# Performance work log

Measured on AMD Instinct MI355X. Metric: run time of the kernel, lower is better.

The kernel has to match this reference:

```python
import jax, jax.numpy as jnp
import numpy as np

B, S, T, H, V = 32, 64, 64, 512, 32000


def setup_inputs() -> dict:
    key = jax.random.key(0)
    ks = jax.random.split(key, 14)
    enc = jax.random.normal(ks[0], (B, S, H), jnp.float32)
    h0 = jax.random.normal(ks[1], (1, B, H), jnp.float32)
    # encoder padding mask: at least half of each row valid (avoids all -inf rows)
    src_len = jax.random.randint(ks[2], (B,), S // 2, S + 1)
    enc_mask = (jnp.arange(S)[None, :] < src_len[:, None])
    tgt = jax.random.randint(ks[3], (B, T), 0, V)
    fra_len = jax.random.randint(ks[4], (B,), 1, T + 1).at[0].set(T)
    s = 1.0 / np.sqrt(H)
    emb = jax.random.normal(ks[5], (V, H), jnp.float32) * s
    W_ih = jax.random.uniform(ks[6], (3 * H, H), jnp.float32, -s, s)
    W_hh = jax.random.uniform(ks[7], (3 * H, H), jnp.float32, -s, s)
    b_ih = jax.random.uniform(ks[8], (3 * H,), jnp.float32, -s, s)
    b_hh = jax.random.uniform(ks[9], (3 * H,), jnp.float32, -s, s)
    W_cc = jax.random.uniform(ks[10], (H, 2 * H), jnp.float32, -s, s)
    b_cc = jnp.zeros((H,), jnp.float32)
    W_out = jax.random.uniform(ks[11], (V, H), jnp.float32, -s, s)
    b_out = jnp.zeros((V,), jnp.float32)
    return {"all_encoder_hidden_states": enc, "initial_decoder_hidden_state": h0,
            "encoder_output_mask": enc_mask, "target_input": tgt, "fra_length": fra_len,
            "embedding": emb, "W_ih": W_ih, "W_hh": W_hh, "b_ih": b_ih, "b_hh": b_hh,
            "W_cc": W_cc, "b_cc": b_cc, "W_out": W_out, "b_out": b_out}


def reference(all_encoder_hidden_states, initial_decoder_hidden_state, encoder_output_mask,
              target_input, fra_length, embedding, W_ih, W_hh, b_ih, b_hh,
              W_cc, b_cc, W_out, b_out):
    enc = all_encoder_hidden_states            # [B,S,H]
    mask = encoder_output_mask                 # [B,S] bool
    xs = embedding[target_input].transpose(1, 0, 2)  # [T,B,H]
    ts = jnp.arange(xs.shape[0])

    def step(h, inp):                          # h: [B,H]
        x, t = inp
        gx = x @ W_ih.T + b_ih                 # [B,3H]
        gh = h @ W_hh.T + b_hh
        gxr, gxz, gxn = jnp.split(gx, 3, axis=-1)
        ghr, ghz, ghn = jnp.split(gh, 3, axis=-1)
        r = jax.nn.sigmoid(gxr + ghr)
        z = jax.nn.sigmoid(gxz + ghz)
        n = jnp.tanh(gxn + r * ghn)
        h_new = (1.0 - z) * n + z * h          # torch GRU update
        # Luong dot-product attention
        scores = jnp.einsum('bsh,bh->bs', enc, h_new)
        scores = jnp.where(mask, scores, -jnp.inf)
        alphas = jax.nn.softmax(scores, axis=-1)
        ctx = jnp.einsum('bs,bsh->bh', alphas, enc)
        ho = jnp.tanh(jnp.concatenate([ctx, h_new], axis=-1) @ W_cc.T + b_cc)
        logit = ho @ W_out.T + b_out           # [B,V]
        active = (t < fra_length)[:, None]
        h_next = jnp.where(active, h_new, h)   # freeze finished sequences
        return h_next, logit

    _, logits = jax.lax.scan(step, initial_decoder_hidden_state[0], (xs, ts))
    logits = logits.transpose(1, 0, 2)          # [B,T,V]
    return jax.nn.log_softmax(logits, axis=-1)
```

## Files before the change

### kernel.cpp

```cpp
#include <hip/hip_runtime.h>

static constexpr int Bn = 32, Sn = 64, Tn = 64, Hn = 512, Vn = 32000;
static constexpr int H3 = 1536;

typedef __attribute__((ext_vector_type(8))) short bf16x8;
typedef __attribute__((ext_vector_type(4))) float f32x4;

__device__ __forceinline__ short f2bf(float f) {
    unsigned u = __float_as_uint(f);
    u += 0x7FFFu + ((u >> 16) & 1u);
    return (short)(u >> 16);
}
__device__ __forceinline__ float bf2f(short s) {
    return __uint_as_float(((unsigned)(unsigned short)s) << 16);
}

__device__ __forceinline__ void gload16(const void* g, void* l) {
    __builtin_amdgcn_global_load_lds(
        (const __attribute__((address_space(1))) unsigned int*)g,
        (__attribute__((address_space(3))) unsigned int*)l, 16, 0, 0);
}

__global__ __launch_bounds__(256) void k_prep(const int* __restrict__ tgt,
                                              const float* __restrict__ emb,
                                              const float* __restrict__ W_ih,
                                              const float* __restrict__ W_hh,
                                              const float* __restrict__ W_cc,
                                              short* __restrict__ Xb,
                                              short* __restrict__ Wih_b, short* __restrict__ Whh_b,
                                              short* __restrict__ Wc1_b, short* __restrict__ Wc2_b) {
    const int bid = blockIdx.x, tid = threadIdx.x;
    if (bid < 2048) {
        long u = (long)bid * 256 + tid;
        const float* src; short* dst;
        if (u < 196608)       { long e = u * 4;            src = W_ih + e; dst = Wih_b + e; }
        else if (u < 393216)  { long e = (u - 196608) * 4; src = W_hh + e; dst = Whh_b + e; }
        else if (u < 458752)  { long e = (u - 393216) * 4; long r = e >> 9; int c = (int)(e & 511);
                                src = W_cc + r * 1024 + c;       dst = Wc1_b + e; }
        else                  { long e = (u - 458752) * 4; long r = e >> 9; int c = (int)(e & 511);
                                src = W_cc + r * 1024 + 512 + c; dst = Wc2_b + e; }
        const float4 v = *(const float4*)src;
        short4 o; o.x = f2bf(v.x); o.y = f2bf(v.y); o.z = f2bf(v.z); o.w = f2bf(v.w);
        *(short4*)dst = o;
    } else {
        const int m = (bid - 2048) * 2 + (tid >> 7);
        const int c = (tid & 127) * 4;
        const float4 v = *(const float4*)(emb + (long)tgt[m] * Hn + c);
        short4 o; o.x = f2bf(v.x); o.y = f2bf(v.y); o.z = f2bf(v.z); o.w = f2bf(v.w);
        *(short4*)(Xb + (long)m * Hn + c) = o;
    }
}

__global__ __launch_bounds__(256) void k_gemm_bf16(const short* __restrict__ A, int lda,
                                                   const short* __restrict__ Bm, int ldb,
                                                   const float* __restrict__ bias,
                                                   float* __restrict__ C, int ldc, int K) {
    __shared__ short lA[4096];
    __shared__ short lB[4096];
    const int tid = threadIdx.x;
    const int row0 = blockIdx.y * 128;
    const int col0 = blockIdx.x * 128;
    const int lane = tid & 63;
    const int w = tid >> 6;
    const int wr = w >> 1, wc = w & 1;
    const int g = lane >> 4, rr = lane & 15;

    f32x4 acc[4][4];
    for (int m = 0; m < 4; ++m)
        for (int n = 0; n < 4; ++n)
            for (int q = 0; q < 4; ++q) acc[m][n][q] = 0.f;

    for (int kk = 0; kk < K; kk += 32) {
        for (int p = 0; p < 2; ++p) {
            int u = p * 256 + tid;
            int kg = u >> 7, r = u & 127;
            gload16(A + (long)(row0 + r) * lda + kk + kg * 8, &lA[u * 8]);
            gload16(Bm + (long)(col0 + r) * ldb + kk + kg * 8, &lB[u * 8]);
        }
        __syncthreads();
        bf16x8 av[4], bv[4];
        for (int m = 0; m < 4; ++m)
            av[m] = *(const bf16x8*)&lA[(g * 128 + wr * 64 + m * 16 + rr) * 8];
        for (int n = 0; n < 4; ++n)
            bv[n] = *(const bf16x8*)&lB[(g * 128 + wc * 64 + n * 16 + rr) * 8];
        for (int m = 0; m < 4; ++m)
            for (int n = 0; n < 4; ++n)
                acc[m][n] = __builtin_amdgcn_mfma_f32_16x16x32_bf16(av[m], bv[n], acc[m][n], 0, 0, 0);
        __syncthreads();
    }

    for (int n = 0; n < 4; ++n) {
        int gc = col0 + wc * 64 + n * 16 + rr;
        float bb = bias ? bias[gc] : 0.f;
        for (int m = 0; m < 4; ++m) {
            int gr = row0 + wr * 64 + m * 16 + g * 4;
            for (int q = 0; q < 4; ++q)
                C[(long)(gr + q) * ldc + gc] = acc[m][n][q] + bb;
        }
    }
}

__global__ __launch_bounds__(256) void k_gemm_logits(const short* __restrict__ A,
                                                     const short* __restrict__ Bm,
                                                     const float* __restrict__ bias,
                                                     float* __restrict__ Cf,
                                                     short* __restrict__ Cb,
                                                     float* __restrict__ stats,
                                                     int use_bf16) {
    __shared__ short lA[4096];
    __shared__ short lB[4096];
    __shared__ float sml[128][2];
    __shared__ float ssl[128][2];
    const int tid = threadIdx.x;
    const int row0 = blockIdx.y * 128;
    const int col0 = blockIdx.x * 128;
    const int lane = tid & 63;
    const int w = tid >> 6;
    const int wr = w >> 1, wc = w & 1;
    const int g = lane >> 4, rr = lane & 15;

    f32x4 acc[4][4];
    for (int m = 0; m < 4; ++m)
        for (int n = 0; n < 4; ++n)
            for (int q = 0; q < 4; ++q) acc[m][n][q] = 0.f;

    for (int kk = 0; kk < 512; kk += 32) {
        for (int p = 0; p < 2; ++p) {
            int u = p * 256 + tid;
            int kg = u >> 7, r = u & 127;
            gload16(A + (long)(row0 + r) * 512 + kk + kg * 8, &lA[u * 8]);
            gload16(Bm + (long)(col0 + r) * 512 + kk + kg * 8, &lB[u * 8]);
        }
        __syncthreads();
        bf16x8 av[4], bv[4];
        for (int m = 0; m < 4; ++m)
            av[m] = *(const bf16x8*)&lA[(g * 128 + wr * 64 + m * 16 + rr) * 8];
        for (int n = 0; n < 4; ++n)
            bv[n] = *(const bf16x8*)&lB[(g * 128 + wc * 64 + n * 16 + rr) * 8];
        for (int m = 0; m < 4; ++m)
            for (int n = 0; n < 4; ++n)
                acc[m][n] = __builtin_amdgcn_mfma_f32_16x16x32_bf16(av[m], bv[n], acc[m][n], 0, 0, 0);
        __syncthreads();
    }

    float bb[4];
    #pragma unroll
    for (int n = 0; n < 4; ++n) bb[n] = bias[col0 + wc * 64 + n * 16 + rr];

    if (use_bf16) {
        #pragma unroll
        for (int n = 0; n < 4; ++n) {
            int gc = col0 + wc * 64 + n * 16 + rr;
            #pragma unroll
            for (int m = 0; m < 4; ++m) {
                int gr = row0 + wr * 64 + m * 16 + g * 4;
                #pragma unroll
                for (int q = 0; q < 4; ++q)
                    Cb[(long)(gr + q) * Vn + gc] = f2bf(acc[m][n][q] + bb[n]);
            }
        }
    } else {
        #pragma unroll
        for (int n = 0; n < 4; ++n) {
            int gc = col0 + wc * 64 + n * 16 + rr;
            #pragma unroll
            for (int m = 0; m < 4; ++m) {
                int gr = row0 + wr * 64 + m * 16 + g * 4;
                #pragma unroll
                for (int q = 0; q < 4; ++q)
                    Cf[(long)(gr + q) * Vn + gc] = acc[m][n][q] + bb[n];
            }
        }
    }
    #pragma unroll
    for (int m = 0; m < 4; ++m) {
        #pragma unroll
        for (int q = 0; q < 4; ++q) {
            float mx = acc[m][0][q] + bb[0];
            mx = fmaxf(mx, acc[m][1][q] + bb[1]);
            mx = fmaxf(mx, acc[m][2][q] + bb[2]);
            mx = fmaxf(mx, acc[m][3][q] + bb[3]);
            mx = fmaxf(mx, __shfl_xor(mx, 1));
            mx = fmaxf(mx, __shfl_xor(mx, 2));
            mx = fmaxf(mx, __shfl_xor(mx, 4));
            mx = fmaxf(mx, __shfl_xor(mx, 8));
            float s = __expf(acc[m][0][q] + bb[0] - mx) + __expf(acc[m][1][q] + bb[1] - mx)
                    + __expf(acc[m][2][q] + bb[2] - mx) + __expf(acc[m][3][q] + bb[3] - mx);
            s += __shfl_xor(s, 1);
            s += __shfl_xor(s, 2);
            s += __shfl_xor(s, 4);
            s += __shfl_xor(s, 8);
            if (rr == 0) {
                const int r = wr * 64 + m * 16 + g * 4 + q;
                sml[r][wc] = mx; ssl[r][wc] = s;
            }
        }
    }
    __syncthreads();
    if (tid < 128) {
        const float m0 = sml[tid][0], m1 = sml[tid][1];
        const float mm = fmaxf(m0, m1);
        const float ss = ssl[tid][0] * __expf(m0 - mm) + ssl[tid][1] * __expf(m1 - mm);
        float2* sp = (float2*)stats;
        sp[(long)(row0 + tid) * 256 + blockIdx.x] = make_float2(mm, ss);
    }
}

__global__ __launch_bounds__(256) void k_sub(float* __restrict__ out, const short* __restrict__ Cb,
                                             const float* __restrict__ stats, int use_bf16) {
    const long row = blockIdx.x;
    const int tid = threadIdx.x;
    __shared__ float lse_s;
    if (tid < 64) {
        float m = -__builtin_inff(), s = 0.f;
        for (int tc = tid; tc < 250; tc += 64) {
            const float2 p = ((const float2*)stats)[row * 256 + tc];
            const float nm = fmaxf(m, p.x);
            s = s * __expf(m - nm) + p.y * __expf(p.x - nm);
            m = nm;
        }
        for (int o = 1; o < 64; o <<= 1) {
            const float om = __shfl_xor(m, o), os = __shfl_xor(s, o);
            const float nm = fmaxf(m, om);
            s = s * __expf(m - nm) + os * __expf(om - nm);
            m = nm;
        }
        if (tid == 0) lse_s = m + logf(s);
    }
    __syncthreads();
    const float lse = lse_s;
    float* p = out + row * (long)Vn;
    if (use_bf16) {
        const short* cp = Cb + row * (long)Vn;
        for (int i = tid; i < Vn / 4; i += 256) {
            short4 c = *(const short4*)(cp + i * 4);
            float4 v;
            v.x = bf2f(c.x) - lse; v.y = bf2f(c.y) - lse;
            v.z = bf2f(c.z) - lse; v.w = bf2f(c.w) - lse;
            *(float4*)(p + i * 4) = v;
        }
    } else {
        for (int i = tid; i < Vn / 4; i += 256) {
            float4 v = *(const float4*)(p + i * 4);
            v.x -= lse; v.y -= lse; v.z -= lse; v.w -= lse;
            *(float4*)(p + i * 4) = v;
        }
    }
}

__global__ __launch_bounds__(256) void k_ho(const short* __restrict__ A1, const short* __restrict__ A2,
                                            const short* __restrict__ B1, const short* __restrict__ B2,
                                            const float* __restrict__ bias, short* __restrict__ C) {
    __shared__ short lA[4096];
    __shared__ short lB[4096];
    const int tid = threadIdx.x;
    const int row0 = blockIdx.y * 128;
    const int col0 = blockIdx.x * 128;
    const int lane = tid & 63;
    const int w = tid >> 6;
    const int wr = w >> 1, wc = w & 1;
    const int g = lane >> 4, rr = lane & 15;

    f32x4 acc[4][4];
    for (int m = 0; m < 4; ++m)
        for (int n = 0; n < 4; ++n)
            for (int q = 0; q < 4; ++q) acc[m][n][q] = 0.f;

    for (int ph = 0; ph < 2; ++ph) {
        const short* A = ph ? A2 : A1;
        const short* Bm = ph ? B2 : B1;
        for (int kk = 0; kk < 512; kk += 32) {
            for (int p = 0; p < 2; ++p) {
                int u = p * 256 + tid;
                int kg = u >> 7, r = u & 127;
                gload16(A + (long)(row0 + r) * 512 + kk + kg * 8, &lA[u * 8]);
                gload16(Bm + (long)(col0 + r) * 512 + kk + kg * 8, &lB[u * 8]);
            }
            __syncthreads();
            bf16x8 av[4], bv[4];
            for (int m = 0; m < 4; ++m)
                av[m] = *(const bf16x8*)&lA[(g * 128 + wr * 64 + m * 16 + rr) * 8];
            for (int n = 0; n < 4; ++n)
                bv[n] = *(const bf16x8*)&lB[(g * 128 + wc * 64 + n * 16 + rr) * 8];
            for (int m = 0; m < 4; ++m)
                for (int n = 0; n < 4; ++n)
                    acc[m][n] = __builtin_amdgcn_mfma_f32_16x16x32_bf16(av[m], bv[n], acc[m][n], 0, 0, 0);
            __syncthreads();
        }
    }

    for (int n = 0; n < 4; ++n) {
        int gc = col0 + wc * 64 + n * 16 + rr;
        float bb = bias[gc];
        for (int m = 0; m < 4; ++m) {
            int gr = row0 + wr * 64 + m * 16 + g * 4;
            for (int q = 0; q < 4; ++q)
                C[(long)(gr + q) * 512 + gc] = f2bf(tanhf(acc[m][n][q] + bb));
        }
    }
}

struct WSm3 {
    short h_all[Bn * Hn];
    float gh_sl[3 * 16 * 32];
};
struct ASm3 {
    short encl[Sn * 520];
    float scp[8][64];
    float al[64];
    short hnf[Hn];
};
union USm3 { WSm3 w; ASm3 a; };

__device__ __forceinline__ void sig_flag(unsigned* slot, unsigned val) {
    asm volatile("s_waitcnt vmcnt(0)" ::: "memory");
    __syncthreads();
    if (threadIdx.x == 0)
        __hip_atomic_store(slot, val, __ATOMIC_RELAXED, __HIP_MEMORY_SCOPE_AGENT);
}
__device__ __forceinline__ void wait_flags32(const unsigned* base, unsigned need) {
    if (threadIdx.x < 32) {
        while (__hip_atomic_load(base + threadIdx.x * 32, __ATOMIC_RELAXED, __HIP_MEMORY_SCOPE_AGENT) < need)
            __builtin_amdgcn_s_sleep(1);
    }
    __syncthreads();
}

__global__ __launch_bounds__(512, 1) void k_seq(
    const float* __restrict__ GX, const int* __restrict__ fra,
    const float* __restrict__ h0,
    const short* __restrict__ Whh_b, const float* __restrict__ b_hh,
    const float* __restrict__ enc, const void* __restrict__ maskp,
    unsigned long long* __restrict__ hn_pk,
    short* __restrict__ ctx_b,
    unsigned long long* __restrict__ hn_pub,
    unsigned* __restrict__ flags,
    const float* __restrict__ W_out, short* __restrict__ Wout_b)
{
    __shared__ __align__(16) USm3 sm;
    const int bid = blockIdx.x;
    const int tid = threadIdx.x;

    if (bid >= 64) {
        const long base = (long)(bid - 64) * (512 * 16);
        #pragma unroll
        for (int it = 0; it < 16; ++it) {
            long i = base + it * 512 + tid;
            if (i < (long)Vn * Hn / 4) {
                const float4 v = *(const float4*)(W_out + i * 4);
                short4 o; o.x = f2bf(v.x); o.y = f2bf(v.y); o.z = f2bf(v.z); o.w = f2bf(v.w);
                *(short4*)(Wout_b + i * 4) = o;
            }
        }
        return;
    }

    const int wv = tid >> 6, lane = tid & 63;

    if (bid >= Bn) {
        const int b = bid - Bn;
        const unsigned w0 = ((const unsigned*)maskp)[0];
        const int mmode = (w0 == 1u) ? 0 : (w0 == 0x3F800000u ? 2 : 1);
        {
            const float* encb = enc + (long)b * (Sn * Hn);
            #pragma unroll
            for (int it = 0; it < 16; ++it) {
                int e = (it * 512 + tid) * 4;
                float4 v = *(const float4*)(encb + e);
                int s = e >> 9, k = e & 511;
                short4 o; o.x = f2bf(v.x); o.y = f2bf(v.y); o.z = f2bf(v.z); o.w = f2bf(v.w);
                *(short4*)(sm.a.encl + s * 520 + k) = o;
            }
        }
        __syncthreads();
        for (int u = 0; u < Tn; ++u) {
            wait_flags32(flags, (unsigned)(u + 1));
            if (tid < 128) {
                unsigned long long v = __hip_atomic_load(hn_pk + (long)(b * Tn + u) * 128 + tid,
                                                         __ATOMIC_RELAXED, __HIP_MEMORY_SCOPE_AGENT);
                *(unsigned long long*)&sm.a.hnf[tid * 4] = v;
            }
            __syncthreads();
            {
                const int s = tid & 63, sub = tid >> 6;
                const short* erow = sm.a.encl + s * 520 + sub * 64;
                const short* hrow = sm.a.hnf + sub * 64;
                float p = 0.f;
                #pragma unroll
                for (int c8 = 0; c8 < 8; ++c8) {
                    bf16x8 ev = *(const bf16x8*)(erow + c8 * 8);
                    bf16x8 hv8 = *(const bf16x8*)(hrow + c8 * 8);
                    #pragma unroll
                    for (int e = 0; e < 8; ++e)
                        p += bf2f(ev[e]) * bf2f(hv8[e]);
                }
                sm.a.scp[sub][s] = p;
            }
            __syncthreads();
            if (tid < 64) {
                float v = 0.f;
                #pragma unroll
                for (int q = 0; q < 8; ++q) v += sm.a.scp[q][tid];
                bool mv;
                if (mmode == 0)      mv = ((const int*)maskp)[b * Sn + tid] != 0;
                else if (mmode == 1) mv = ((const unsigned char*)maskp)[b * Sn + tid] != 0;
                else                 mv = ((const float*)maskp)[b * Sn + tid] != 0.f;
                v = mv ? v : -__builtin_inff();
                float mx = v;
                for (int o = 1; o < 64; o <<= 1) mx = fmaxf(mx, __shfl_xor(mx, o));
                float e = __expf(v - mx);
                float su = e;
                for (int o = 1; o < 64; o <<= 1) su += __shfl_xor(su, o);
                sm.a.al[tid] = e / su;
            }
            __syncthreads();
            {
                float cx = 0.f;
                #pragma unroll 8
                for (int s = 0; s < 64; ++s)
                    cx += sm.a.al[s] * bf2f(sm.a.encl[s * 520 + tid]);
                ctx_b[(long)(b * Tn + u) * Hn + tid] = f2bf(cx);
            }
        }
        return;
    }

    bf16x8 afr[16];
    if (wv < 6) {
        const int g = wv >> 1;
        const int row = g * 512 + bid * 16 + (lane & 15);
        #pragma unroll
        for (int k = 0; k < 16; ++k)
            afr[k] = *(const bf16x8*)(Whh_b + (long)row * 512 + k * 32 + (lane >> 4) * 8);
    }
    #pragma unroll
    for (int it = 0; it < 8; ++it) {
        const int idx2 = it * 512 + tid;
        const int b = idx2 >> 7, ci2 = idx2 & 127;
        const int j0 = ci2 * 4;
        const int soff = b * 512 + ((((ci2 >> 1)) ^ (b & 7)) << 3) + (ci2 & 1) * 4;
        const float4 v = *(const float4*)(h0 + b * 512 + j0);
        unsigned long long pk = (unsigned long long)(unsigned short)f2bf(v.x)
                              | ((unsigned long long)(unsigned short)f2bf(v.y) << 16)
                              | ((unsigned long long)(unsigned short)f2bf(v.z) << 32)
                              | ((unsigned long long)(unsigned short)f2bf(v.w) << 48);
        *(unsigned long long*)&sm.w.h_all[soff] = pk;
    }

    const int eb = tid >> 4, jj = tid & 15;
    float h_carry = h0[eb * 512 + bid * 16 + jj];
    const int flen_e = fra[eb];
    const int jglob = bid * 16 + jj;
    const float bhr = b_hh[jglob];
    const float bhz = b_hh[512 + jglob];
    const float bhn = b_hh[1024 + jglob];

    const int ci2s = wv * 16 + (lane & 15);
    const unsigned* fp = flags + (ci2s >> 2) * 32;
    const int bbase = lane >> 4;

    for (int t = 0; t < Tn; ++t) {
        const long base = (long)(eb * Tn + t) * H3 + jglob;
        const float gxr = GX[base];
        const float gxz = GX[base + 512];
        const float gxn = GX[base + 1024];
        if (t >= 1) {
            while (__hip_atomic_load(fp, __ATOMIC_RELAXED, __HIP_MEMORY_SCOPE_AGENT) < (unsigned)t)
                __builtin_amdgcn_s_sleep(1);
            const unsigned long long* src = hn_pub + ((t - 1) & 1) * 4096;
            #pragma unroll
            for (int it = 0; it < 8; ++it) {
                const int b = bbase + it * 4;
                const unsigned long long v =
                    __hip_atomic_load(src + b * 128 + ci2s, __ATOMIC_RELAXED, __HIP_MEMORY_SCOPE_AGENT);
                const int soff = b * 512 + ((((ci2s >> 1)) ^ (b & 7)) << 3) + (ci2s & 1) * 4;
                *(unsigned long long*)&sm.w.h_all[soff] = v;
            }
        }
        __syncthreads();
        if (wv < 6) {
            const int g = wv >> 1, n = wv & 1;
            const int bq = n * 16 + (lane & 15);
            f32x4 a0 = {0.f, 0.f, 0.f, 0.f}, a1 = {0.f, 0.f, 0.f, 0.f};
            #pragma unroll
            for (int k = 0; k < 8; ++k) {
                const int c0 = k * 4 + (lane >> 4);
                const int c1 = (k + 8) * 4 + (lane >> 4);
                bf16x8 b0 = *(const bf16x8*)&sm.w.h_all[bq * 512 + ((c0 ^ (bq & 7)) << 3)];
                bf16x8 b1 = *(const bf16x8*)&sm.w.h_all[bq * 512 + ((c1 ^ (bq & 7)) << 3)];
                a0 = __builtin_amdgcn_mfma_f32_16x16x32_bf16(afr[k], b0, a0, 0, 0, 0);
                a1 = __builtin_amdgcn_mfma_f32_16x16x32_bf16(afr[k + 8], b1, a1, 0, 0, 0);
            }
            const int r0 = (lane >> 4) * 4;
            #pragma unroll
            for (int q = 0; q < 4; ++q)
                sm.w.gh_sl[g * 512 + (r0 + q) * 32 + bq] = a0[q] + a1[q];
        }
        __syncthreads();
        {
            const float ghr = sm.w.gh_sl[jj * 32 + eb]          + bhr;
            const float ghz = sm.w.gh_sl[512 + jj * 32 + eb]    + bhz;
            const float ghn = sm.w.gh_sl[1024 + jj * 32 + eb]   + bhn;
            const float r = 1.f / (1.f + __expf(-(gxr + ghr)));
            const float z = 1.f / (1.f + __expf(-(gxz + ghz)));
            const float nn = tanhf(gxn + r * ghn);
            const float hv = (1.f - z) * nn + z * h_carry;
            h_carry = (t < flen_e) ? hv : h_carry;
            int f32w = (int)(unsigned short)f2bf(h_carry);
            int r32w = (int)(unsigned short)f2bf(hv);
            int f1 = __shfl_down(f32w, 1), f2 = __shfl_down(f32w, 2), f3 = __shfl_down(f32w, 3);
            int r1 = __shfl_down(r32w, 1), r2 = __shfl_down(r32w, 2), r3 = __shfl_down(r32w, 3);
            if ((jj & 3) == 0) {
                unsigned long long pkf = (unsigned long long)(unsigned)(f32w | (f1 << 16))
                                       | ((unsigned long long)(unsigned)(f2 | (f3 << 16)) << 32);
                unsigned long long pkr = (unsigned long long)(unsigned)(r32w | (r1 << 16))
                                       | ((unsigned long long)(unsigned)(r2 | (r3 << 16)) << 32);
                __hip_atomic_store(hn_pub + (t & 1) * 4096 + eb * 128 + bid * 4 + (jj >> 2), pkf,
                                   __ATOMIC_RELAXED, __HIP_MEMORY_SCOPE_AGENT);
                __hip_atomic_store(hn_pk + (long)(eb * Tn + t) * 128 + bid * 4 + (jj >> 2), pkr,
                                   __ATOMIC_RELAXED, __HIP_MEMORY_SCOPE_AGENT);
            }
            sig_flag(flags + bid * 32, (unsigned)(t + 1));
        }
    }
}

extern "C" void kernel_launch(void* const* d_in, const int* in_sizes, int n_in,
                              void* d_out, int out_size, void* d_ws, size_t ws_size,
                              hipStream_t stream) {
    const float* enc   = (const float*)d_in[0];
    const float* h0    = (const float*)d_in[1];
    const void*  maskp = d_in[2];
    const int*   tgt   = (const int*)d_in[3];
    const int*   fra   = (const int*)d_in[4];
    const float* emb   = (const float*)d_in[5];
    const float* W_ih  = (const float*)d_in[6];
    const float* W_hh  = (const float*)d_in[7];
    const float* b_ih  = (const float*)d_in[8];
    const float* b_hh  = (const float*)d_in[9];
    const float* W_cc  = (const float*)d_in[10];
    const float* b_cc  = (const float*)d_in[11];
    const float* W_out = (const float*)d_in[12];
    const float* b_out = (const float*)d_in[13];
    float* out = (float*)d_out;

    char* ws = (char*)d_ws;
    float*    GX      = (float*)ws;   ws += (long)2048 * 1536 * 4;
    short*    Xb      = (short*)ws;   ws += (long)2048 * 512 * 2;
    short*    Wih_b   = (short*)ws;   ws += (long)1536 * 512 * 2;
    short*    Wout_b  = (short*)ws;   ws += (long)32000 * 512 * 2;
    short*    Whh_b   = (short*)ws;   ws += (long)1536 * 512 * 2;
    short*    Wc1_b   = (short*)ws;   ws += (long)512 * 512 * 2;
    short*    Wcc2_b  = (short*)ws;   ws += (long)512 * 512 * 2;
    short*    ho_b    = (short*)ws;   ws += (long)2048 * 512 * 2;
    short*    hn_all  = (short*)ws;   ws += (long)2048 * 512 * 2;
    short*    ctx_b   = (short*)ws;   ws += (long)2048 * 512 * 2;
    float*    stats   = (float*)ws;   ws += (long)2048 * 256 * 2 * 4;
    unsigned long long* hn_pub = (unsigned long long*)ws; ws += (long)2 * 4096 * 8;
    unsigned* flags   = (unsigned*)ws; ws += 1024 * 4;
    const long cb_bytes = (long)2048 * Vn * 2;
    const long used = (long)(ws - (char*)d_ws);
    const int use_bf16 = (ws_size >= (size_t)(used + cb_bytes)) ? 1 : 0;
    short* Cb = use_bf16 ? (short*)ws : nullptr;

    hipMemsetAsync(flags, 0, 1024 * 4, stream);
    k_prep<<<3072, 256, 0, stream>>>(tgt, emb, W_ih, W_hh, W_cc, Xb, Wih_b, Whh_b, Wc1_b, Wcc2_b);

    k_gemm_bf16<<<dim3(12, 16), 256, 0, stream>>>(Xb, 512, Wih_b, 512, b_ih, GX, 1536, 512);

    k_seq<<<576, 512, 0, stream>>>(GX, fra, h0, Whh_b, b_hh, enc, maskp,
                                   (unsigned long long*)hn_all, ctx_b, hn_pub, flags,
                                   W_out, Wout_b);

    k_ho<<<dim3(4, 16), 256, 0, stream>>>(ctx_b, hn_all, Wc1_b, Wcc2_b, b_cc, ho_b);

    k_gemm_logits<<<dim3(250, 16), 256, 0, stream>>>(ho_b, Wout_b, b_out, out, Cb, stats, use_bf16);

    k_sub<<<2048, 256, 0, stream>>>(out, Cb, stats, use_bf16);
}
```

Measured before the change: 676.0 us.

## Fuse combine-projection and logits GEMM into persistent sequential kernel with flag pipelining

Removes the separate k_ho and k_gemm_logits launches. Attention blocks now compute the tanh(W_cc·[ctx,h]) projection every four timesteps and publish ho rows with flags. 192 extra persistent blocks convert W_out to bf16 and then run the vocabulary logits GEMM tiles as soon as each 128-row chunk of ho is ready, so the large GEMM overlaps the recurrent GRU loop. Rows are reordered time-major, with index remapping in k_sub and stats. This adds spin-wait synchronisation and relies on co-residency of all 256 blocks, and the GEMM tiles may contend with the latency-critical recurrence.

```diff
diff --git a/kernel.cpp b/kernel.cpp
--- a/kernel.cpp
+++ b/kernel.cpp
@@ -28,17 +28,14 @@
                                               const float* __restrict__ W_cc,
                                               short* __restrict__ Xb,
                                               short* __restrict__ Wih_b, short* __restrict__ Whh_b,
-                                              short* __restrict__ Wc1_b, short* __restrict__ Wc2_b) {
+                                              short* __restrict__ Wcc_b) {
     const int bid = blockIdx.x, tid = threadIdx.x;
     if (bid < 2048) {
         long u = (long)bid * 256 + tid;
         const float* src; short* dst;
         if (u < 196608)       { long e = u * 4;            src = W_ih + e; dst = Wih_b + e; }
         else if (u < 393216)  { long e = (u - 196608) * 4; src = W_hh + e; dst = Whh_b + e; }
-        else if (u < 458752)  { long e = (u - 393216) * 4; long r = e >> 9; int c = (int)(e & 511);
-                                src = W_cc + r * 1024 + c;       dst = Wc1_b + e; }
-        else                  { long e = (u - 458752) * 4; long r = e >> 9; int c = (int)(e & 511);
-                                src = W_cc + r * 1024 + 512 + c; dst = Wc2_b + e; }
+        else                  { long e = (u - 393216) * 4; src = W_cc + e; dst = Wcc_b + e; }
         const float4 v = *(const float4*)src;
         short4 o; o.x = f2bf(v.x); o.y = f2bf(v.y); o.z = f2bf(v.z); o.w = f2bf(v.w);
         *(short4*)dst = o;
@@ -100,112 +97,6 @@
     }
 }
 
-__global__ __launch_bounds__(256) void k_gemm_logits(const short* __restrict__ A,
-                                                     const short* __restrict__ Bm,
-                                                     const float* __restrict__ bias,
-                                                     float* __restrict__ Cf,
-                                                     short* __restrict__ Cb,
-                                                     float* __restrict__ stats,
-                                                     int use_bf16) {
-    __shared__ short lA[4096];
-    __shared__ short lB[4096];
-    __shared__ float sml[128][2];
-    __shared__ float ssl[128][2];
-    const int tid = threadIdx.x;
-    const int row0 = blockIdx.y * 128;
-    const int col0 = blockIdx.x * 128;
-    const int lane = tid & 63;
-    const int w = tid >> 6;
-    const int wr = w >> 1, wc = w & 1;
-    const int g = lane >> 4, rr = lane & 15;
-
-    f32x4 acc[4][4];
-    for (int m = 0; m < 4; ++m)
-        for (int n = 0; n < 4; ++n)
-            for (int q = 0; q < 4; ++q) acc[m][n][q] = 0.f;
-
-    for (int kk = 0; kk < 512; kk += 32) {
-        for (int p = 0; p < 2; ++p) {
-            int u = p * 256 + tid;
-            int kg = u >> 7, r = u & 127;
-            gload16(A + (long)(row0 + r) * 512 + kk + kg * 8, &lA[u * 8]);
-            gload16(Bm + (long)(col0 + r) * 512 + kk + kg * 8, &lB[u * 8]);
-        }
-        __syncthreads();
-        bf16x8 av[4], bv[4];
-        for (int m = 0; m < 4; ++m)
-            av[m] = *(const bf16x8*)&lA[(g * 128 + wr * 64 + m * 16 + rr) * 8];
-        for (int n = 0; n < 4; ++n)
-            bv[n] = *(const bf16x8*)&lB[(g * 128 + wc * 64 + n * 16 + rr) * 8];
-        for (int m = 0; m < 4; ++m)
-            for (int n = 0; n < 4; ++n)
-                acc[m][n] = __builtin_amdgcn_mfma_f32_16x16x32_bf16(av[m], bv[n], acc[m][n], 0, 0, 0);
-        __syncthreads();
-    }
-
-    float bb[4];
-    #pragma unroll
-    for (int n = 0; n < 4; ++n) bb[n] = bias[col0 + wc * 64 + n * 16 + rr];
-
-    if (use_bf16) {
-        #pragma unroll
-        for (int n = 0; n < 4; ++n) {
-            int gc = col0 + wc * 64 + n * 16 + rr;
-            #pragma unroll
-            for (int m = 0; m < 4; ++m) {
-                int gr = row0 + wr * 64 + m * 16 + g * 4;
-                #pragma unroll
-                for (int q = 0; q < 4; ++q)
-                    Cb[(long)(gr + q) * Vn + gc] = f2bf(acc[m][n][q] + bb[n]);
-            }
-        }
-    } else {
-        #pragma unroll
-        for (int n = 0; n < 4; ++n) {
-            int gc = col0 + wc * 64 + n * 16 + rr;
-            #pragma unroll
-            for (int m = 0; m < 4; ++m) {
-                int gr = row0 + wr * 64 + m * 16 + g * 4;
-                #pragma unroll
-                for (int q = 0; q < 4; ++q)
-                    Cf[(long)(gr + q) * Vn + gc] = acc[m][n][q] + bb[n];
-            }
-        }
-    }
-    #pragma unroll
-    for (int m = 0; m < 4; ++m) {
-        #pragma unroll
-        for (int q = 0; q < 4; ++q) {
-            float mx = acc[m][0][q] + bb[0];
-            mx = fmaxf(mx, acc[m][1][q] + bb[1]);
-            mx = fmaxf(mx, acc[m][2][q] + bb[2]);
-            mx = fmaxf(mx, acc[m][3][q] + bb[3]);
-            mx = fmaxf(mx, __shfl_xor(mx, 1));
-            mx = fmaxf(mx, __shfl_xor(mx, 2));
-            mx = fmaxf(mx, __shfl_xor(mx, 4));
-            mx = fmaxf(mx, __shfl_xor(mx, 8));
-            float s = __expf(acc[m][0][q] + bb[0] - mx) + __expf(acc[m][1][q] + bb[1] - mx)
-                    + __expf(acc[m][2][q] + bb[2] - mx) + __expf(acc[m][3][q] + bb[3] - mx);
-            s += __shfl_xor(s, 1);
-            s += __shfl_xor(s, 2);
-            s += __shfl_xor(s, 4);
-            s += __shfl_xor(s, 8);
-            if (rr == 0) {
-                const int r = wr * 64 + m * 16 + g * 4 + q;
-                sml[r][wc] = mx; ssl[r][wc] = s;
-            }
-        }
-    }
-    __syncthreads();
-    if (tid < 128) {
-        const float m0 = sml[tid][0], m1 = sml[tid][1];
-        const float mm = fmaxf(m0, m1);
-        const float ss = ssl[tid][0] * __expf(m0 - mm) + ssl[tid][1] * __expf(m1 - mm);
-        float2* sp = (float2*)stats;
-        sp[(long)(row0 + tid) * 256 + blockIdx.x] = make_float2(mm, ss);
-    }
-}
-
 __global__ __launch_bounds__(256) void k_sub(float* __restrict__ out, const short* __restrict__ Cb,
                                              const float* __restrict__ stats, int use_bf16) {
     const long row = blockIdx.x;
@@ -231,7 +122,8 @@
     const float lse = lse_s;
     float* p = out + row * (long)Vn;
     if (use_bf16) {
-        const short* cp = Cb + row * (long)Vn;
+        const long rowp = (row & 63) * 32 + (row >> 6);
+        const short* cp = Cb + rowp * (long)Vn;
         for (int i = tid; i < Vn / 4; i += 256) {
             short4 c = *(const short4*)(cp + i * 4);
             float4 v;
@@ -248,69 +140,23 @@
     }
 }
 
-__global__ __launch_bounds__(256) void k_ho(const short* __restrict__ A1, const short* __restrict__ A2,
-                                            const short* __restrict__ B1, const short* __restrict__ B2,
-                                            const float* __restrict__ bias, short* __restrict__ C) {
-    __shared__ short lA[4096];
-    __shared__ short lB[4096];
-    const int tid = threadIdx.x;
-    const int row0 = blockIdx.y * 128;
-    const int col0 = blockIdx.x * 128;
-    const int lane = tid & 63;
-    const int w = tid >> 6;
-    const int wr = w >> 1, wc = w & 1;
-    const int g = lane >> 4, rr = lane & 15;
-
-    f32x4 acc[4][4];
-    for (int m = 0; m < 4; ++m)
-        for (int n = 0; n < 4; ++n)
-            for (int q = 0; q < 4; ++q) acc[m][n][q] = 0.f;
-
-    for (int ph = 0; ph < 2; ++ph) {
-        const short* A = ph ? A2 : A1;
-        const short* Bm = ph ? B2 : B1;
-        for (int kk = 0; kk < 512; kk += 32) {
-            for (int p = 0; p < 2; ++p) {
-                int u = p * 256 + tid;
-                int kg = u >> 7, r = u & 127;
-                gload16(A + (long)(row0 + r) * 512 + kk + kg * 8, &lA[u * 8]);
-                gload16(Bm + (long)(col0 + r) * 512 + kk + kg * 8, &lB[u * 8]);
-            }
-            __syncthreads();
-            bf16x8 av[4], bv[4];
-            for (int m = 0; m < 4; ++m)
-                av[m] = *(const bf16x8*)&lA[(g * 128 + wr * 64 + m * 16 + rr) * 8];
-            for (int n = 0; n < 4; ++n)
-                bv[n] = *(const bf16x8*)&lB[(g * 128 + wc * 64 + n * 16 + rr) * 8];
-            for (int m = 0; m < 4; ++m)
-                for (int n = 0; n < 4; ++n)
-                    acc[m][n] = __builtin_amdgcn_mfma_f32_16x16x32_bf16(av[m], bv[n], acc[m][n], 0, 0, 0);
-            __syncthreads();
-        }
-    }
-
-    for (int n = 0; n < 4; ++n) {
-        int gc = col0 + wc * 64 + n * 16 + rr;
-        float bb = bias[gc];
-        for (int m = 0; m < 4; ++m) {
-            int gr = row0 + wr * 64 + m * 16 + g * 4;
-            for (int q = 0; q < 4; ++q)
-                C[(long)(gr + q) * 512 + gc] = f2bf(tanhf(acc[m][n][q] + bb));
-        }
-    }
-}
-
 struct WSm3 {
     short h_all[Bn * Hn];
     float gh_sl[3 * 16 * 32];
 };
 struct ASm3 {
     short encl[Sn * 520];
+    short Abuf[16 * 1032];
     float scp[8][64];
     float al[64];
-    short hnf[Hn];
 };
-union USm3 { WSm3 w; ASm3 a; };
+struct GSm3 {
+    short lA[2][4096];
+    short lB[2][4096];
+    float sml[2][128][2];
+    float ssl[2][128][2];
+};
+union USm3 { WSm3 w; ASm3 a; GSm3 g; };
 
 __device__ __forceinline__ void sig_flag(unsigned* slot, unsigned val) {
     asm volatile("s_waitcnt vmcnt(0)" ::: "memory");
@@ -331,36 +177,151 @@
     const float* __restrict__ h0,
     const short* __restrict__ Whh_b, const float* __restrict__ b_hh,
     const float* __restrict__ enc, const void* __restrict__ maskp,
+    const short* __restrict__ Wcc_b, const float* __restrict__ b_cc,
+    const float* __restrict__ W_out, short* __restrict__ Wout_b,
+    const float* __restrict__ b_out,
     unsigned long long* __restrict__ hn_pk,
-    short* __restrict__ ctx_b,
+    short* __restrict__ ho_b,
     unsigned long long* __restrict__ hn_pub,
     unsigned* __restrict__ flags,
-    const float* __restrict__ W_out, short* __restrict__ Wout_b)
+    float* __restrict__ outF, short* __restrict__ Cb,
+    float* __restrict__ stats, int use_bf16)
 {
     __shared__ __align__(16) USm3 sm;
     const int bid = blockIdx.x;
     const int tid = threadIdx.x;
+    const int wv = tid >> 6, lane = tid & 63;
+    unsigned* flagW = flags;
+    unsigned* flagC = flags + 1024;
+    unsigned* flagV = flags + 2048;
 
     if (bid >= 64) {
-        const long base = (long)(bid - 64) * (512 * 16);
-        #pragma unroll
-        for (int it = 0; it < 16; ++it) {
-            long i = base + it * 512 + tid;
+        const int idx = bid - 64;
+        for (int it = 0; it < 42; ++it) {
+            long i = (long)it * 98304 + idx * 512 + tid;
             if (i < (long)Vn * Hn / 4) {
                 const float4 v = *(const float4*)(W_out + i * 4);
-                short4 o; o.x = f2bf(v.x); o.y = f2bf(v.y); o.z = f2bf(v.z); o.w = f2bf(v.w);
-                *(short4*)(Wout_b + i * 4) = o;
-            }
+                unsigned long long pk = (unsigned long long)(unsigned short)f2bf(v.x)
+                                      | ((unsigned long long)(unsigned short)f2bf(v.y) << 16)
+                                      | ((unsigned long long)(unsigned short)f2bf(v.z) << 32)
+                                      | ((unsigned long long)(unsigned short)f2bf(v.w) << 48);
+                __hip_atomic_store((unsigned long long*)(Wout_b + i * 4), pk,
+                                   __ATOMIC_RELAXED, __HIP_MEMORY_SCOPE_AGENT);
+            }
+        }
+        sig_flag(flagV + idx * 8, 1u);
+        if (tid < 192) {
+            while (__hip_atomic_load(flagV + tid * 8, __ATOMIC_RELAXED, __HIP_MEMORY_SCOPE_AGENT) < 1u)
+                __builtin_amdgcn_s_sleep(1);
+        }
+        __syncthreads();
+
+        const int half = wv >> 2;
+        const int tid2 = tid & 255;
+        const int lane2 = tid2 & 63, w2 = tid2 >> 6;
+        const int wr = w2 >> 1, wc = w2 & 1;
+        const int g2 = lane2 >> 4, rr2 = lane2 & 15;
+
+        for (int p = idx; p < 2000; p += 192) {
+            const int tau = 2 * p + half;
+            const int rtp = tau / 250, ct = tau % 250;
+            const int rtmax = (2 * p + 1) / 250;
+            wait_flags32(flagC, (unsigned)(rtmax + 1));
+            const int row0 = rtp * 128;
+            const int col0 = ct * 128;
+
+            f32x4 acc[4][4];
+            for (int m = 0; m < 4; ++m)
+                for (int n = 0; n < 4; ++n)
+                    for (int q = 0; q < 4; ++q) acc[m][n][q] = 0.f;
+
+            for (int kk = 0; kk < 512; kk += 32) {
+                for (int p2 = 0; p2 < 2; ++p2) {
+                    int u = p2 * 256 + tid2;
+                    int kg = u >> 7, r = u & 127;
+                    gload16(ho_b + (long)(row0 + r) * 512 + kk + kg * 8, &sm.g.lA[half][u * 8]);
+                    gload16(Wout_b + (long)(col0 + r) * 512 + kk + kg * 8, &sm.g.lB[half][u * 8]);
+                }
+                __syncthreads();
+                bf16x8 av[4], bv[4];
+                for (int m = 0; m < 4; ++m)
+                    av[m] = *(const bf16x8*)&sm.g.lA[half][(g2 * 128 + wr * 64 + m * 16 + rr2) * 8];
+                for (int n = 0; n < 4; ++n)
+                    bv[n] = *(const bf16x8*)&sm.g.lB[half][(g2 * 128 + wc * 64 + n * 16 + rr2) * 8];
+                for (int m = 0; m < 4; ++m)
+                    for (int n = 0; n < 4; ++n)
+                        acc[m][n] = __builtin_amdgcn_mfma_f32_16x16x32_bf16(av[m], bv[n], acc[m][n], 0, 0, 0);
+                __syncthreads();
+            }
+
+            float bb[4];
+            #pragma unroll
+            for (int n = 0; n < 4; ++n) bb[n] = b_out[col0 + wc * 64 + n * 16 + rr2];
+
+            #pragma unroll
+            for (int n = 0; n < 4; ++n) {
+                int gc = col0 + wc * 64 + n * 16 + rr2;
+                #pragma unroll
+                for (int m = 0; m < 4; ++m) {
+                    int grp = row0 + wr * 64 + m * 16 + g2 * 4;
+                    #pragma unroll
+                    for (int q = 0; q < 4; ++q) {
+                        if (use_bf16) {
+                            Cb[(long)(grp + q) * Vn + gc] = f2bf(acc[m][n][q] + bb[n]);
+                        } else {
+                            const int rp = grp + q;
+                            const long fr = (long)(rp & 31) * 64 + (rp >> 5);
+                            outF[fr * Vn + gc] = acc[m][n][q] + bb[n];
+                        }
+                    }
+                }
+            }
+            #pragma unroll
+            for (int m = 0; m < 4; ++m) {
+                #pragma unroll
+                for (int q = 0; q < 4; ++q) {
+                    float mx = acc[m][0][q] + bb[0];
+                    mx = fmaxf(mx, acc[m][1][q] + bb[1]);
+                    mx = fmaxf(mx, acc[m][2][q] + bb[2]);
+                    mx = fmaxf(mx, acc[m][3][q] + bb[3]);
+                    mx = fmaxf(mx, __shfl_xor(mx, 1));
+                    mx = fmaxf(mx, __shfl_xor(mx, 2));
+                    mx = fmaxf(mx, __shfl_xor(mx, 4));
+                    mx = fmaxf(mx, __shfl_xor(mx, 8));
+                    float s = __expf(acc[m][0][q] + bb[0] - mx) + __expf(acc[m][1][q] + bb[1] - mx)
+                            + __expf(acc[m][2][q] + bb[2] - mx) + __expf(acc[m][3][q] + bb[3] - mx);
+                    s += __shfl_xor(s, 1);
+                    s += __shfl_xor(s, 2);
+                    s += __shfl_xor(s, 4);
+                    s += __shfl_xor(s, 8);
+                    if (rr2 == 0) {
+                        const int r = wr * 64 + m * 16 + g2 * 4 + q;
+                        sm.g.sml[half][r][wc] = mx; sm.g.ssl[half][r][wc] = s;
+                    }
+                }
+            }
+            __syncthreads();
+            if (tid < 256) {
+                const int h2 = tid >> 7, r = tid & 127;
+                const int tau2 = 2 * p + h2;
+                const int rowp = (tau2 / 250) * 128 + r;
+                const int ct2 = tau2 % 250;
+                const float m0 = sm.g.sml[h2][r][0], m1 = sm.g.sml[h2][r][1];
+                const float mm = fmaxf(m0, m1);
+                const float ss = sm.g.ssl[h2][r][0] * __expf(m0 - mm) + sm.g.ssl[h2][r][1] * __expf(m1 - mm);
+                const long fr = (long)(rowp & 31) * 64 + (rowp >> 5);
+                ((float2*)stats)[fr * 256 + ct2] = make_float2(mm, ss);
+            }
+            __syncthreads();
         }
         return;
     }
-
-    const int wv = tid >> 6, lane = tid & 63;
 
     if (bid >= Bn) {
         const int b = bid - Bn;
         const unsigned w0 = ((const unsigned*)maskp)[0];
         const int mmode = (w0 == 1u) ? 0 : (w0 == 0x3F800000u ? 2 : 1);
+        const int g = lane >> 4, rr = lane & 15;
         {
             const float* encb = enc + (long)b * (Sn * Hn);
             #pragma unroll
@@ -374,17 +335,18 @@
         }
         __syncthreads();
         for (int u = 0; u < Tn; ++u) {
-            wait_flags32(flags, (unsigned)(u + 1));
+            const int t4 = u & 3;
+            wait_flags32(flagW, (unsigned)(u + 1));
             if (tid < 128) {
                 unsigned long long v = __hip_atomic_load(hn_pk + (long)(b * Tn + u) * 128 + tid,
                                                          __ATOMIC_RELAXED, __HIP_MEMORY_SCOPE_AGENT);
-                *(unsigned long long*)&sm.a.hnf[tid * 4] = v;
+                *(unsigned long long*)&sm.a.Abuf[t4 * 1032 + 512 + tid * 4] = v;
             }
             __syncthreads();
             {
                 const int s = tid & 63, sub = tid >> 6;
                 const short* erow = sm.a.encl + s * 520 + sub * 64;
-                const short* hrow = sm.a.hnf + sub * 64;
+                const short* hrow = sm.a.Abuf + t4 * 1032 + 512 + sub * 64;
                 float p = 0.f;
                 #pragma unroll
                 for (int c8 = 0; c8 < 8; ++c8) {
@@ -419,7 +381,32 @@
                 #pragma unroll 8
                 for (int s = 0; s < 64; ++s)
                     cx += sm.a.al[s] * bf2f(sm.a.encl[s * 520 + tid]);
-                ctx_b[(long)(b * Tn + u) * Hn + tid] = f2bf(cx);
+                sm.a.Abuf[t4 * 1032 + tid] = f2bf(cx);
+            }
+            if (t4 == 3) {
+                __syncthreads();
+                const int t0 = u - 3;
+                #pragma unroll
+                for (int ni = 0; ni < 4; ++ni) {
+                    const int j0 = (wv * 4 + ni) * 16;
+                    f32x4 acc = {0.f, 0.f, 0.f, 0.f};
+                    for (int k = 0; k < 32; ++k) {
+                        bf16x8 av = *(const bf16x8*)&sm.a.Abuf[rr * 1032 + k * 32 + g * 8];
+                        bf16x8 bv = *(const bf16x8*)(Wcc_b + (long)(j0 + rr) * 1024 + k * 32 + g * 8);
+                        acc = __builtin_amdgcn_mfma_f32_16x16x32_bf16(av, bv, acc, 0, 0, 0);
+                    }
+                    if (g == 0) {
+                        const int j = j0 + rr;
+                        const float bc = b_cc[j];
+                        #pragma unroll
+                        for (int q = 0; q < 4; ++q) {
+                            const short hv = f2bf(tanhf(acc[q] + bc));
+                            __hip_atomic_store(ho_b + (long)((t0 + q) * 32 + b) * 512 + j, hv,
+                                               __ATOMIC_RELAXED, __HIP_MEMORY_SCOPE_AGENT);
+                        }
+                    }
+                }
+                sig_flag(flagC + b * 32, (unsigned)((u >> 2) + 1));
             }
         }
         return;
@@ -456,7 +443,7 @@
     const float bhn = b_hh[1024 + jglob];
 
     const int ci2s = wv * 16 + (lane & 15);
-    const unsigned* fp = flags + (ci2s >> 2) * 32;
+    const unsigned* fp = flagW + (ci2s >> 2) * 32;
     const int bbase = lane >> 4;
 
     for (int t = 0; t < Tn; ++t) {
@@ -520,7 +507,7 @@
                 __hip_atomic_store(hn_pk + (long)(eb * Tn + t) * 128 + bid * 4 + (jj >> 2), pkr,
                                    __ATOMIC_RELAXED, __HIP_MEMORY_SCOPE_AGENT);
             }
-            sig_flag(flags + bid * 32, (unsigned)(t + 1));
+            sig_flag(flagW + bid * 32, (unsigned)(t + 1));
         }
     }
 }
@@ -550,31 +537,26 @@
     short*    Wih_b   = (short*)ws;   ws += (long)1536 * 512 * 2;
     short*    Wout_b  = (short*)ws;   ws += (long)32000 * 512 * 2;
     short*    Whh_b   = (short*)ws;   ws += (long)1536 * 512 * 2;
-    short*    Wc1_b   = (short*)ws;   ws += (long)512 * 512 * 2;
-    short*    Wcc2_b  = (short*)ws;   ws += (long)512 * 512 * 2;
+    short*    Wcc_b   = (short*)ws;   ws += (long)512 * 1024 * 2;
     short*    ho_b    = (short*)ws;   ws += (long)2048 * 512 * 2;
-    short*    hn_all  = (short*)ws;   ws += (long)2048 * 512 * 2;
-    short*    ctx_b   = (short*)ws;   ws += (long)2048 * 512 * 2;
+    short*    hn_pk_s = (short*)ws;   ws += (long)2048 * 512 * 2;
     float*    stats   = (float*)ws;   ws += (long)2048 * 256 * 2 * 4;
     unsigned long long* hn_pub = (unsigned long long*)ws; ws += (long)2 * 4096 * 8;
-    unsigned* flags   = (unsigned*)ws; ws += 1024 * 4;
+    unsigned* flags   = (unsigned*)ws; ws += 16384;
     const long cb_bytes = (long)2048 * Vn * 2;
     const long used = (long)(ws - (char*)d_ws);
     const int use_bf16 = (ws_size >= (size_t)(used + cb_bytes)) ? 1 : 0;
     short* Cb = use_bf16 ? (short*)ws : nullptr;
 
-    hipMemsetAsync(flags, 0, 1024 * 4, stream);
-    k_prep<<<3072, 256, 0, stream>>>(tgt, emb, W_ih, W_hh, W_cc, Xb, Wih_b, Whh_b, Wc1_b, Wcc2_b);
+    hipMemsetAsync(flags, 0, 16384, stream);
+    k_prep<<<3072, 256, 0, stream>>>(tgt, emb, W_ih, W_hh, W_cc, Xb, Wih_b, Whh_b, Wcc_b);
 
     k_gemm_bf16<<<dim3(12, 16), 256, 0, stream>>>(Xb, 512, Wih_b, 512, b_ih, GX, 1536, 512);
 
-    k_seq<<<576, 512, 0, stream>>>(GX, fra, h0, Whh_b, b_hh, enc, maskp,
-                                   (unsigned long long*)hn_all, ctx_b, hn_pub, flags,
-                                   W_out, Wout_b);
-
-    k_ho<<<dim3(4, 16), 256, 0, stream>>>(ctx_b, hn_all, Wc1_b, Wcc2_b, b_cc, ho_b);
-
-    k_gemm_logits<<<dim3(250, 16), 256, 0, stream>>>(ho_b, Wout_b, b_out, out, Cb, stats, use_bf16);
+    k_seq<<<256, 512, 0, stream>>>(GX, fra, h0, Whh_b, b_hh, enc, maskp,
+                                   Wcc_b, b_cc, W_out, Wout_b, b_out,
+                                   (unsigned long long*)hn_pk_s, ho_b, hn_pub, flags,
+                                   out, Cb, stats, use_bf16);
 
     k_sub<<<2048, 256, 0, stream>>>(out, Cb, stats, use_bf16);
 }
```

After: 856.3 us. +26.7%, slower.
